# Performance work log

Hardware: AMD Instinct MI355X
Metric: run time of the kernel (lower is better)

Reference implementation:

```python
import jax, jax.numpy as jnp
import numpy as np

B, T, D = 4, 2048, 2048
P, K, ALPHA, R = 512, 16, 4, 32
E_RATIO = 0.8
EPS = 1e-6


def rmsnorm(x, g):
    return x * jax.lax.rsqrt(jnp.mean(x * x, axis=-1, keepdims=True) + EPS) * g


def dale_signs():
    # first e_ratio*P neurons excitatory (+1), rest inhibitory (-1)
    return jnp.where(jnp.arange(P) < int(E_RATIO * P), 1.0, -1.0)


def quant_dale(w, signs):
    # STE sign-quantization with per-neuron mean-abs scale + Dale's-law sign constraint
    scale = jnp.mean(jnp.abs(w), axis=-1, keepdims=True)  # [P,1]
    q = scale * signs[:, None] * jnp.ones_like(w)         # magnitude=scale, sign fixed per neuron
    return w + jax.lax.stop_gradient(q - w)


def synapse_graph(x, idx, w):
    # x: [B,T,D], idx: [P,K] int, w: [P,K] -> dendritic inputs [B,T,P,K]
    return jnp.take(x, idx, axis=-1) * w


def perceptron(x_dend, Wp, Wout, signs):
    Wq = quant_dale(Wp, signs)                              # [P,K]
    u = jnp.einsum('btpk,pk->btp', x_dend, Wq)              # [B,T,P]
    f = jax.nn.sigmoid(u)                                   # gate [B,T,P]
    f_out = quant_dale(Wout, signs)                         # [P,ALPHA]
    y = (f * u)[..., None] * f_out                          # [B,T,P,ALPHA]
    return u, f, y, f_out


def low_rank_ssm(t, f, s0, U, V, Wgate, bgate):
    # t,f: [B,T,P]; s0: [B,R]. Low-rank gated linear scan in R dims.
    z = jnp.einsum('btp,pr->btr', t, U)
    lam = jax.nn.sigmoid(jnp.einsum('btp,pr->btr', f, Wgate) + bgate)

    def step(s, inp):
        z_t, l_t = inp
        s = l_t * s + z_t
        return s, s

    sT, S = jax.lax.scan(step, s0, (jnp.moveaxis(z, 1, 0), jnp.moveaxis(lam, 1, 0)))
    tilde = jnp.einsum('btr,rp->btp', jnp.moveaxis(S, 0, 1), V)
    return tilde, sT


def flatten_ports(y):
    return y.reshape(*y.shape[:-2], P * ALPHA)


def setup_inputs() -> dict:
    key = jax.random.key(0)
    ks = jax.random.split(key, 14)
    sc = 0.1
    return {
        'x': jax.random.normal(ks[0], (B, T, D), jnp.float32),
        'state': jnp.zeros((B, R), jnp.float32),
        'g1': jnp.ones((D,), jnp.float32),
        'g2': jnp.ones((D,), jnp.float32),
        'idx_ssm': jax.random.randint(ks[1], (P, K), 0, D),
        'wg_ssm': jax.random.normal(ks[2], (P, K), jnp.float32) * sc,
        'idx_mlp': jax.random.randint(ks[3], (P, K), 0, D),
        'wg_mlp': jax.random.normal(ks[4], (P, K), jnp.float32) * sc,
        'Wp_ssm': jax.random.normal(ks[5], (P, K), jnp.float32) * sc,
        'Wout_ssm': jax.random.normal(ks[6], (P, ALPHA), jnp.float32) * sc,
        'Wp_mlp': jax.random.normal(ks[7], (P, K), jnp.float32) * sc,
        'Wout_mlp': jax.random.normal(ks[8], (P, ALPHA), jnp.float32) * sc,
        'U': jax.random.normal(ks[9], (P, R), jnp.float32) * sc,
        'V': jax.random.normal(ks[10], (R, P), jnp.float32) * sc,
        'Wgate': jax.random.normal(ks[11], (P, R), jnp.float32) * sc,
        'bgate': jnp.zeros((R,), jnp.float32),
    }


def reference(x, state, g1, g2, idx_ssm, wg_ssm, idx_mlp, wg_mlp,
              Wp_ssm, Wout_ssm, Wp_mlp, Wout_mlp, U, V, Wgate, bgate):
    signs = dale_signs()
    # --- SSM branch ---
    h1 = rmsnorm(x, g1)
    x_dend_ssm = synapse_graph(h1, idx_ssm, wg_ssm)
    u_ssm, f_ssm, _, f_out = perceptron(x_dend_ssm, Wp_ssm, Wout_ssm, signs)
    t_ssm = f_ssm * u_ssm
    tilde_t, new_state = low_rank_ssm(t_ssm, f_ssm, state, U, V, Wgate, bgate)
    y_ssm = (f_ssm * tilde_t)[..., None] * f_out            # [B,T,P,ALPHA]
    x_after = x + flatten_ports(y_ssm)
    # --- MLP branch ---
    h2 = rmsnorm(x_after, g2)
    x_dend_mlp = synapse_graph(h2, idx_mlp, wg_mlp)
    _, _, y_mlp, _ = perceptron(x_dend_mlp, Wp_mlp, Wout_mlp, signs)
    x_out = x_after + flatten_ports(y_mlp)
    return x_out, new_state
```

## Files before the change

kernel.cpp:

```cpp
#include <hip/hip_runtime.h>
#include <hip/hip_bf16.h>

#define B_ 4
#define T_ 2048
#define D_ 2048
#define P_ 512
#define K_ 16
#define ALPHA_ 4
#define R_ 32
#define NE_ 409
#define EPS_ 1e-6f
#define G_ 4

typedef unsigned short u16;
typedef unsigned int u32;
typedef _Float16 h2t __attribute__((ext_vector_type(2)));

__device__ __forceinline__ float sigmoidf_(float x) {
  return 1.0f / (1.0f + __expf(-x));
}
__device__ __forceinline__ float bfb2f(u16 u) {
  return __uint_as_float(((u32)u) << 16);
}
__device__ __forceinline__ u16 f2bfb(float f) {
  __hip_bfloat16 h = __float2bfloat16(f);
  return *reinterpret_cast<u16*>(&h);
}
__device__ __forceinline__ u32 packh(float lo, float hi) {
#if __has_builtin(__builtin_amdgcn_cvt_pkrtz)
  return __builtin_bit_cast(u32, __builtin_amdgcn_cvt_pkrtz(lo, hi));
#else
  union { _Float16 h; u16 u; } a, b;
  a.h = (_Float16)lo; b.h = (_Float16)hi;
  return ((u32)b.u << 16) | a.u;
#endif
}
__device__ __forceinline__ u32 duph(float w) {
  union { _Float16 h; u16 u; } c;
  c.h = (_Float16)w;
  return ((u32)c.u << 16) | c.u;
}
__device__ __forceinline__ h2t pkfma(u32 h, u32 w, h2t acc) {
  return __builtin_bit_cast(h2t, h) * __builtin_bit_cast(h2t, w) + acc;
}

__global__ void k_scalars(const float* __restrict__ Wp_s, const float* __restrict__ Wo_s,
                          const float* __restrict__ Wp_m, const float* __restrict__ Wo_m,
                          const float* __restrict__ U, const float* __restrict__ Wgt,
                          const float* __restrict__ wg_s, const float* __restrict__ wg_m,
                          float* __restrict__ wq_s, float* __restrict__ fo_s,
                          float* __restrict__ wq_m, float* __restrict__ fo_m,
                          u32* __restrict__ Ud, u32* __restrict__ Wd,
                          u32* __restrict__ wgd_s, u32* __restrict__ wgd_m) {
  int p = blockIdx.x * blockDim.x + threadIdx.x;
  if (p >= P_) return;
  float sgn = (p < NE_) ? 1.0f : -1.0f;
  float a = 0, b = 0, c = 0, d = 0;
#pragma unroll
  for (int k = 0; k < K_; k++) {
    a += fabsf(Wp_s[p * K_ + k]);
    c += fabsf(Wp_m[p * K_ + k]);
  }
#pragma unroll
  for (int k = 0; k < ALPHA_; k++) {
    b += fabsf(Wo_s[p * ALPHA_ + k]);
    d += fabsf(Wo_m[p * ALPHA_ + k]);
  }
  wq_s[p] = sgn * a * (1.0f / K_);
  fo_s[p] = sgn * b * (1.0f / ALPHA_);
  wq_m[p] = sgn * c * (1.0f / K_);
  fo_m[p] = sgn * d * (1.0f / ALPHA_);
#pragma unroll
  for (int r = 0; r < R_; r++) {
    Ud[p * R_ + r] = duph(U[p * R_ + r]);
    Wd[p * R_ + r] = duph(Wgt[p * R_ + r]);
  }
#pragma unroll
  for (int k = 0; k < K_; k++) {
    wgd_s[p * K_ + k] = duph(wg_s[p * K_ + k]);
    wgd_m[p * K_ + k] = duph(wg_m[p * K_ + k]);
  }
}

__global__ __launch_bounds__(512) void k_phase1(
    const float* __restrict__ x, const float* __restrict__ g1,
    const int* __restrict__ idx, const u32* __restrict__ wgd,
    const u32* __restrict__ Ud, const u32* __restrict__ Wd,
    const float* __restrict__ bg, const float* __restrict__ wq,
    u16* __restrict__ f_ssm, float* __restrict__ z, float* __restrict__ lam) {
  __shared__ union SU {
    u32 h1p[2][D_];
    struct { float zp[G_][R_][8]; float lp[G_][R_][8]; } c;
  } su;
  __shared__ u32 tp[2][P_];
  __shared__ u32 fp[2][P_];
  __shared__ float red[G_][8];

  int tid = threadIdx.x;
  int token0 = blockIdx.x * G_;
  int b = token0 >> 11;
  int t0 = token0 & (T_ - 1);

  float gv[4];
  *reinterpret_cast<float4*>(gv) = *reinterpret_cast<const float4*>(g1 + tid * 4);
#pragma unroll
  for (int pr = 0; pr < 2; pr++) {
    int ta = 2 * pr, tb = ta + 1;
    float xv0[4], xv1[4];
    *reinterpret_cast<float4*>(xv0) =
        *reinterpret_cast<const float4*>(x + (size_t)(token0 + ta) * D_ + tid * 4);
    *reinterpret_cast<float4*>(xv1) =
        *reinterpret_cast<const float4*>(x + (size_t)(token0 + tb) * D_ + tid * 4);
    float ss0 = 0, ss1 = 0;
    u32 tmp[4];
#pragma unroll
    for (int i = 0; i < 4; i++) {
      ss0 += xv0[i] * xv0[i];
      ss1 += xv1[i] * xv1[i];
      tmp[i] = packh(xv0[i] * gv[i], xv1[i] * gv[i]);
    }
    *reinterpret_cast<uint4*>(&su.h1p[pr][tid * 4]) = *reinterpret_cast<const uint4*>(tmp);
#pragma unroll
    for (int off = 32; off; off >>= 1) {
      ss0 += __shfl_down(ss0, off);
      ss1 += __shfl_down(ss1, off);
    }
    if ((tid & 63) == 0) { red[ta][tid >> 6] = ss0; red[tb][tid >> 6] = ss1; }
  }
  __syncthreads();

  float inv[G_];
#pragma unroll
  for (int tok = 0; tok < G_; tok++) {
    float s = 0;
#pragma unroll
    for (int w = 0; w < 8; w++) s += red[tok][w];
    inv[tok] = rsqrtf(s * (1.0f / D_) + EPS_);
  }

  {
    int p = tid;
    union { int4 v[4]; int s[16]; } iu;
    const int4* ip = reinterpret_cast<const int4*>(idx + p * K_);
    iu.v[0] = ip[0]; iu.v[1] = ip[1]; iu.v[2] = ip[2]; iu.v[3] = ip[3];
    union { uint4 v[4]; u32 s[16]; } wd;
    const uint4* wp = reinterpret_cast<const uint4*>(wgd + p * K_);
    wd.v[0] = wp[0]; wd.v[1] = wp[1]; wd.v[2] = wp[2]; wd.v[3] = wp[3];
    float wqp = wq[p];
#pragma unroll
    for (int pr = 0; pr < 2; pr++) {
      int ta = 2 * pr, tb = ta + 1;
      h2t acc = {(_Float16)0.0f, (_Float16)0.0f};
#pragma unroll
      for (int k = 0; k < K_; k++) acc = pkfma(su.h1p[pr][iu.s[k]], wd.s[k], acc);
      float u0 = wqp * inv[ta] * (float)acc.x, u1 = wqp * inv[tb] * (float)acc.y;
      float f0 = sigmoidf_(u0), f1 = sigmoidf_(u1);
      tp[pr][p] = packh(f0 * u0, f1 * u1);
      fp[pr][p] = packh(f0, f1);
      f_ssm[(size_t)(token0 + ta) * P_ + p] = f2bfb(f0);
      f_ssm[(size_t)(token0 + tb) * P_ + p] = f2bfb(f1);
    }
  }
  __syncthreads();

  int r = tid & 31, g = tid >> 5;
  float zs[G_] = {0, 0, 0, 0}, ls[G_] = {0, 0, 0, 0};
  int pb = g * 32;
#pragma unroll
  for (int c = 0; c < 4; c++) {
    h2t z0 = {(_Float16)0.0f, (_Float16)0.0f}, z1 = z0, l0 = z0, l1 = z0;
#pragma unroll
    for (int i = 0; i < 8; i++) {
      int p = pb + c * 8 + i;
      u32 ud = Ud[p * R_ + r];
      u32 wdd = Wd[p * R_ + r];
      z0 = pkfma(tp[0][p], ud, z0);
      z1 = pkfma(tp[1][p], ud, z1);
      l0 = pkfma(fp[0][p], wdd, l0);
      l1 = pkfma(fp[1][p], wdd, l1);
    }
    zs[0] += (float)z0.x; zs[1] += (float)z0.y; zs[2] += (float)z1.x; zs[3] += (float)z1.y;
    ls[0] += (float)l0.x; ls[1] += (float)l0.y; ls[2] += (float)l1.x; ls[3] += (float)l1.y;
  }
#pragma unroll
  for (int tok = 0; tok < G_; tok++) {
    zs[tok] += __shfl_down(zs[tok], 32);
    ls[tok] += __shfl_down(ls[tok], 32);
  }
  int wid = tid >> 6;
  if ((tid & 63) < 32) {
#pragma unroll
    for (int tok = 0; tok < G_; tok++) { su.c.zp[tok][r][wid] = zs[tok]; su.c.lp[tok][r][wid] = ls[tok]; }
  }
  __syncthreads();
  if (tid < R_) {
    float bgr = bg[tid];
    float z4[G_], l4[G_];
#pragma unroll
    for (int tok = 0; tok < G_; tok++) {
      float zz = 0, ll = 0;
#pragma unroll
      for (int w = 0; w < 8; w++) { zz += su.c.zp[tok][tid][w]; ll += su.c.lp[tok][tid][w]; }
      z4[tok] = zz;
      l4[tok] = sigmoidf_(ll + bgr);
    }
    size_t o = ((size_t)(b * R_ + tid)) * T_ + t0;
    *reinterpret_cast<float4*>(&z[o]) = *reinterpret_cast<const float4*>(z4);
    *reinterpret_cast<float4*>(&lam[o]) = *reinterpret_cast<const float4*>(l4);
  }
}

__global__ __launch_bounds__(64) void k_scan(
    const float* __restrict__ z, const float* __restrict__ lam,
    const float* __restrict__ state, float* __restrict__ S,
    float* __restrict__ out_state) {
  int br = blockIdx.x;
  int lane = threadIdx.x;
  const float* zr = z + (size_t)br * T_ + lane * 32;
  const float* lr = lam + (size_t)br * T_ + lane * 32;
  float zb[32], lb[32];
#pragma unroll
  for (int i = 0; i < 32; i += 4) {
    *reinterpret_cast<float4*>(&zb[i]) = *reinterpret_cast<const float4*>(&zr[i]);
    *reinterpret_cast<float4*>(&lb[i]) = *reinterpret_cast<const float4*>(&lr[i]);
  }
  float A = 1.0f, Z = 0.0f;
#pragma unroll
  for (int i = 0; i < 32; i++) { Z = lb[i] * Z + zb[i]; A *= lb[i]; }
  for (int off = 1; off < 64; off <<= 1) {
    float Ap = __shfl_up(A, off);
    float Zp = __shfl_up(Z, off);
    if (lane >= off) { Z = A * Zp + Z; A = A * Ap; }
  }
  float s0 = state[br];
  float Ae = __shfl_up(A, 1);
  float Ze = __shfl_up(Z, 1);
  float s = (lane == 0) ? s0 : (Ae * s0 + Ze);
  float sb[32];
#pragma unroll
  for (int i = 0; i < 32; i++) { s = lb[i] * s + zb[i]; sb[i] = s; }
  float* Sr = S + (size_t)br * T_ + lane * 32;
#pragma unroll
  for (int i = 0; i < 32; i += 4)
    *reinterpret_cast<float4*>(&Sr[i]) = *reinterpret_cast<const float4*>(&sb[i]);
  if (lane == 63) out_state[br] = s;
}

__global__ __launch_bounds__(512) void k_phase3(
    const float* __restrict__ x, const float* __restrict__ g2,
    const int* __restrict__ idx, const u32* __restrict__ wgd,
    const float* __restrict__ V, const float* __restrict__ S,
    const u16* __restrict__ f_ssm, const float* __restrict__ fo_s,
    const float* __restrict__ wq_m, const float* __restrict__ fo_m,
    float* __restrict__ out) {
  __shared__ float Sl[G_][R_];
  __shared__ u32 h2p[2][D_];
  __shared__ float red[G_][8];

  int tid = threadIdx.x;
  int token0 = blockIdx.x * G_;
  int b = token0 >> 11;
  int t0 = token0 & (T_ - 1);
  int p = tid;

  if (tid < G_ * R_) {
    int tok = tid >> 5, r = tid & 31;
    Sl[tok][r] = S[((size_t)(b * R_ + r)) * T_ + t0 + tok];
  }
  __syncthreads();

  float til[G_] = {0, 0, 0, 0};
#pragma unroll 4
  for (int r = 0; r < R_; r++) {
    float v = V[r * P_ + p];
#pragma unroll
    for (int tok = 0; tok < G_; tok++) til[tok] += Sl[tok][r] * v;
  }

  float fo = fo_s[p];
  float gv[4];
  *reinterpret_cast<float4*>(gv) = *reinterpret_cast<const float4*>(g2 + tid * 4);

  float xa[G_][4];
#pragma unroll
  for (int pr = 0; pr < 2; pr++) {
    int ta = 2 * pr, tb = ta + 1;
#pragma unroll
    for (int h = 0; h < 2; h++) {
      int tok = ta + h;
      float fv = bfb2f(f_ssm[(size_t)(token0 + tok) * P_ + p]);
      float val = fv * til[tok] * fo;
      float xv[4];
      *reinterpret_cast<float4*>(xv) =
          *reinterpret_cast<const float4*>(x + (size_t)(token0 + tok) * D_ + tid * 4);
      float ss = 0;
#pragma unroll
      for (int a = 0; a < 4; a++) {
        float v = xv[a] + val;
        xa[tok][a] = v;
        ss += v * v;
      }
#pragma unroll
      for (int off = 32; off; off >>= 1) ss += __shfl_down(ss, off);
      if ((tid & 63) == 0) red[tok][tid >> 6] = ss;
    }
    u32 tmp[4];
#pragma unroll
    for (int i = 0; i < 4; i++)
      tmp[i] = packh(xa[ta][i] * gv[i], xa[tb][i] * gv[i]);
    *reinterpret_cast<uint4*>(&h2p[pr][tid * 4]) = *reinterpret_cast<const uint4*>(tmp);
  }
  __syncthreads();

  float invt[G_];
#pragma unroll
  for (int tok = 0; tok < G_; tok++) {
    float s = 0;
#pragma unroll
    for (int w = 0; w < 8; w++) s += red[tok][w];
    invt[tok] = rsqrtf(s * (1.0f / D_) + EPS_);
  }

  union { int4 v[4]; int s[16]; } iu;
  union { uint4 v[4]; u32 s[16]; } wd;
  {
    const int4* ip = reinterpret_cast<const int4*>(idx + p * K_);
    const uint4* wp = reinterpret_cast<const uint4*>(wgd + p * K_);
#pragma unroll
    for (int q = 0; q < 4; q++) { iu.v[q] = ip[q]; wd.v[q] = wp[q]; }
  }
  float wqm = wq_m[p];
  float fom = fo_m[p];

#pragma unroll
  for (int pr = 0; pr < 2; pr++) {
    h2t acc = {(_Float16)0.0f, (_Float16)0.0f};
#pragma unroll
    for (int k = 0; k < K_; k++) acc = pkfma(h2p[pr][iu.s[k]], wd.s[k], acc);
#pragma unroll
    for (int h = 0; h < 2; h++) {
      int tok = 2 * pr + h;
      float a = h ? (float)acc.y : (float)acc.x;
      float u = wqm * invt[tok] * a;
      float f = sigmoidf_(u);
      float val = f * u * fom;
      float ov[4];
#pragma unroll
      for (int a2 = 0; a2 < 4; a2++) ov[a2] = xa[tok][a2] + val;
      *reinterpret_cast<float4*>(out + (size_t)(token0 + tok) * D_ + tid * 4) =
          *reinterpret_cast<const float4*>(ov);
    }
  }
}

extern "C" void kernel_launch(void* const* d_in, const int* in_sizes, int n_in,
                              void* d_out, int out_size, void* d_ws, size_t ws_size,
                              hipStream_t stream) {
  const float* x     = (const float*)d_in[0];
  const float* state = (const float*)d_in[1];
  const float* g1    = (const float*)d_in[2];
  const float* g2    = (const float*)d_in[3];
  const int*   idx_s = (const int*)d_in[4];
  const float* wg_s  = (const float*)d_in[5];
  const int*   idx_m = (const int*)d_in[6];
  const float* wg_m  = (const float*)d_in[7];
  const float* Wp_s  = (const float*)d_in[8];
  const float* Wo_s  = (const float*)d_in[9];
  const float* Wp_m  = (const float*)d_in[10];
  const float* Wo_m  = (const float*)d_in[11];
  const float* U     = (const float*)d_in[12];
  const float* V     = (const float*)d_in[13];
  const float* Wgt   = (const float*)d_in[14];
  const float* bg    = (const float*)d_in[15];
  float* out = (float*)d_out;

  char* ws = (char*)d_ws;
  float* wq_s = (float*)(ws + 0);
  float* fo_s = (float*)(ws + 2048);
  float* wq_m = (float*)(ws + 4096);
  float* fo_m = (float*)(ws + 6144);
  u32* Ud     = (u32*)(ws + 8192);
  u32* Wd     = (u32*)(ws + 8192 + 65536);
  u32* wgd_s  = (u32*)(ws + 8192 + 131072);
  u32* wgd_m  = (u32*)(ws + 8192 + 163840);
  size_t off = 8192 + 196608;
  u16* f_ssm = (u16*)(ws + off); off += (size_t)B_ * T_ * P_ * 2;
  float* z   = (float*)(ws + off); off += (size_t)B_ * R_ * T_ * 4;
  float* lam = (float*)(ws + off); off += (size_t)B_ * R_ * T_ * 4;
  float* S   = (float*)(ws + off);

  hipLaunchKernelGGL(k_scalars, dim3(2), dim3(256), 0, stream,
                     Wp_s, Wo_s, Wp_m, Wo_m, U, Wgt, wg_s, wg_m,
                     wq_s, fo_s, wq_m, fo_m, Ud, Wd, wgd_s, wgd_m);
  hipLaunchKernelGGL(k_phase1, dim3(B_ * T_ / G_), dim3(512), 0, stream,
                     x, g1, idx_s, wgd_s, Ud, Wd, bg, wq_s, f_ssm, z, lam);
  hipLaunchKernelGGL(k_scan, dim3(B_ * R_), dim3(64), 0, stream,
                     z, lam, state, S, out + (size_t)B_ * T_ * D_);
  hipLaunchKernelGGL(k_phase3, dim3(B_ * T_ / G_), dim3(512), 0, stream,
                     x, g2, idx_m, wgd_m, V, S, f_ssm, fo_s, wq_m, fo_m, out);
}
```

Baseline: 207.6 us.

## Store f_ssm as packed fp16 pairs, hoist index loads, vectorize LDS reads

The SSM gate f is now stored as one packed fp16 pair per token pair (one 32-bit store) instead of two scattered bf16 stores, and phase3 reads it back as a single word. Index and scale loads are hoisted to kernel start in both phases so their latency overlaps the RMSnorm reductions. The low-rank projection reads tp/fp from LDS with 128-bit loads, and both kernels get a min-blocks launch bound. The aim is fewer global transactions and better latency hiding. The costs are fp16 rounding of f instead of bf16 and added register pressure from the bound.

After: 223.3 us. +7.6%, slower.

```diff
diff --git a/kernel.cpp b/kernel.cpp
--- a/kernel.cpp
+++ b/kernel.cpp
@@ -19,13 +19,6 @@
 __device__ __forceinline__ float sigmoidf_(float x) {
   return 1.0f / (1.0f + __expf(-x));
 }
-__device__ __forceinline__ float bfb2f(u16 u) {
-  return __uint_as_float(((u32)u) << 16);
-}
-__device__ __forceinline__ u16 f2bfb(float f) {
-  __hip_bfloat16 h = __float2bfloat16(f);
-  return *reinterpret_cast<u16*>(&h);
-}
 __device__ __forceinline__ u32 packh(float lo, float hi) {
 #if __has_builtin(__builtin_amdgcn_cvt_pkrtz)
   return __builtin_bit_cast(u32, __builtin_amdgcn_cvt_pkrtz(lo, hi));
@@ -35,6 +28,8 @@
   return ((u32)b.u << 16) | a.u;
 #endif
 }
+__device__ __forceinline__ float hlo(u32 u) { return (float)__builtin_bit_cast(h2t, u).x; }
+__device__ __forceinline__ float hhi(u32 u) { return (float)__builtin_bit_cast(h2t, u).y; }
 __device__ __forceinline__ u32 duph(float w) {
   union { _Float16 h; u16 u; } c;
   c.h = (_Float16)w;
@@ -82,12 +77,12 @@
   }
 }
 
-__global__ __launch_bounds__(512) void k_phase1(
+__global__ __launch_bounds__(512, 8) void k_phase1(
     const float* __restrict__ x, const float* __restrict__ g1,
     const int* __restrict__ idx, const u32* __restrict__ wgd,
     const u32* __restrict__ Ud, const u32* __restrict__ Wd,
     const float* __restrict__ bg, const float* __restrict__ wq,
-    u16* __restrict__ f_ssm, float* __restrict__ z, float* __restrict__ lam) {
+    u32* __restrict__ f_ssm, float* __restrict__ z, float* __restrict__ lam) {
   __shared__ union SU {
     u32 h1p[2][D_];
     struct { float zp[G_][R_][8]; float lp[G_][R_][8]; } c;
@@ -100,6 +95,13 @@
   int token0 = blockIdx.x * G_;
   int b = token0 >> 11;
   int t0 = token0 & (T_ - 1);
+
+  union { int4 v[4]; int s[16]; } iu;
+  {
+    const int4* ip = reinterpret_cast<const int4*>(idx + tid * K_);
+    iu.v[0] = ip[0]; iu.v[1] = ip[1]; iu.v[2] = ip[2]; iu.v[3] = ip[3];
+  }
+  float wqp = wq[tid];
 
   float gv[4];
   *reinterpret_cast<float4*>(gv) = *reinterpret_cast<const float4*>(g1 + tid * 4);
@@ -140,13 +142,9 @@
 
   {
     int p = tid;
-    union { int4 v[4]; int s[16]; } iu;
-    const int4* ip = reinterpret_cast<const int4*>(idx + p * K_);
-    iu.v[0] = ip[0]; iu.v[1] = ip[1]; iu.v[2] = ip[2]; iu.v[3] = ip[3];
     union { uint4 v[4]; u32 s[16]; } wd;
     const uint4* wp = reinterpret_cast<const uint4*>(wgd + p * K_);
     wd.v[0] = wp[0]; wd.v[1] = wp[1]; wd.v[2] = wp[2]; wd.v[3] = wp[3];
-    float wqp = wq[p];
 #pragma unroll
     for (int pr = 0; pr < 2; pr++) {
       int ta = 2 * pr, tb = ta + 1;
@@ -156,9 +154,9 @@
       float u0 = wqp * inv[ta] * (float)acc.x, u1 = wqp * inv[tb] * (float)acc.y;
       float f0 = sigmoidf_(u0), f1 = sigmoidf_(u1);
       tp[pr][p] = packh(f0 * u0, f1 * u1);
-      fp[pr][p] = packh(f0, f1);
-      f_ssm[(size_t)(token0 + ta) * P_ + p] = f2bfb(f0);
-      f_ssm[(size_t)(token0 + tb) * P_ + p] = f2bfb(f1);
+      u32 fpk = packh(f0, f1);
+      fp[pr][p] = fpk;
+      f_ssm[(size_t)(2 * blockIdx.x + pr) * P_ + p] = fpk;
     }
   }
   __syncthreads();
@@ -170,14 +168,20 @@
   for (int c = 0; c < 4; c++) {
     h2t z0 = {(_Float16)0.0f, (_Float16)0.0f}, z1 = z0, l0 = z0, l1 = z0;
 #pragma unroll
-    for (int i = 0; i < 8; i++) {
-      int p = pb + c * 8 + i;
-      u32 ud = Ud[p * R_ + r];
-      u32 wdd = Wd[p * R_ + r];
-      z0 = pkfma(tp[0][p], ud, z0);
-      z1 = pkfma(tp[1][p], ud, z1);
-      l0 = pkfma(fp[0][p], wdd, l0);
-      l1 = pkfma(fp[1][p], wdd, l1);
+    for (int q = 0; q < 2; q++) {
+      int p = pb + c * 8 + q * 4;
+      uint4 t0 = *reinterpret_cast<const uint4*>(&tp[0][p]);
+      uint4 t1 = *reinterpret_cast<const uint4*>(&tp[1][p]);
+      uint4 f0 = *reinterpret_cast<const uint4*>(&fp[0][p]);
+      uint4 f1 = *reinterpret_cast<const uint4*>(&fp[1][p]);
+      u32 u0 = Ud[(p + 0) * R_ + r], u1 = Ud[(p + 1) * R_ + r];
+      u32 u2 = Ud[(p + 2) * R_ + r], u3 = Ud[(p + 3) * R_ + r];
+      u32 w0 = Wd[(p + 0) * R_ + r], w1 = Wd[(p + 1) * R_ + r];
+      u32 w2 = Wd[(p + 2) * R_ + r], w3 = Wd[(p + 3) * R_ + r];
+      z0 = pkfma(t0.w, u3, pkfma(t0.z, u2, pkfma(t0.y, u1, pkfma(t0.x, u0, z0))));
+      z1 = pkfma(t1.w, u3, pkfma(t1.z, u2, pkfma(t1.y, u1, pkfma(t1.x, u0, z1))));
+      l0 = pkfma(f0.w, w3, pkfma(f0.z, w2, pkfma(f0.y, w1, pkfma(f0.x, w0, l0))));
+      l1 = pkfma(f1.w, w3, pkfma(f1.z, w2, pkfma(f1.y, w1, pkfma(f1.x, w0, l1))));
     }
     zs[0] += (float)z0.x; zs[1] += (float)z0.y; zs[2] += (float)z1.x; zs[3] += (float)z1.y;
     ls[0] += (float)l0.x; ls[1] += (float)l0.y; ls[2] += (float)l1.x; ls[3] += (float)l1.y;
@@ -246,11 +250,11 @@
   if (lane == 63) out_state[br] = s;
 }
 
-__global__ __launch_bounds__(512) void k_phase3(
+__global__ __launch_bounds__(512, 8) void k_phase3(
     const float* __restrict__ x, const float* __restrict__ g2,
     const int* __restrict__ idx, const u32* __restrict__ wgd,
     const float* __restrict__ V, const float* __restrict__ S,
-    const u16* __restrict__ f_ssm, const float* __restrict__ fo_s,
+    const u32* __restrict__ f_ssm, const float* __restrict__ fo_s,
     const float* __restrict__ wq_m, const float* __restrict__ fo_m,
     float* __restrict__ out) {
   __shared__ float Sl[G_][R_];
@@ -263,6 +267,16 @@
   int t0 = token0 & (T_ - 1);
   int p = tid;
 
+  union { int4 v[4]; int s[16]; } iu;
+  {
+    const int4* ip = reinterpret_cast<const int4*>(idx + p * K_);
+    iu.v[0] = ip[0]; iu.v[1] = ip[1]; iu.v[2] = ip[2]; iu.v[3] = ip[3];
+  }
+  u32 fw[2];
+#pragma unroll
+  for (int pr = 0; pr < 2; pr++)
+    fw[pr] = f_ssm[(size_t)(2 * blockIdx.x + pr) * P_ + p];
+
   if (tid < G_ * R_) {
     int tok = tid >> 5, r = tid & 31;
     Sl[tok][r] = S[((size_t)(b * R_ + r)) * T_ + t0 + tok];
@@ -288,7 +302,7 @@
 #pragma unroll
     for (int h = 0; h < 2; h++) {
       int tok = ta + h;
-      float fv = bfb2f(f_ssm[(size_t)(token0 + tok) * P_ + p]);
+      float fv = h ? hhi(fw[pr]) : hlo(fw[pr]);
       float val = fv * til[tok] * fo;
       float xv[4];
       *reinterpret_cast<float4*>(xv) =
@@ -321,13 +335,11 @@
     invt[tok] = rsqrtf(s * (1.0f / D_) + EPS_);
   }
 
-  union { int4 v[4]; int s[16]; } iu;
   union { uint4 v[4]; u32 s[16]; } wd;
   {
-    const int4* ip = reinterpret_cast<const int4*>(idx + p * K_);
     const uint4* wp = reinterpret_cast<const uint4*>(wgd + p * K_);
 #pragma unroll
-    for (int q = 0; q < 4; q++) { iu.v[q] = ip[q]; wd.v[q] = wp[q]; }
+    for (int q = 0; q < 4; q++) wd.v[q] = wp[q];
   }
   float wqm = wq_m[p];
   float fom = fo_m[p];
@@ -384,7 +396,7 @@
   u32* wgd_s  = (u32*)(ws + 8192 + 131072);
   u32* wgd_m  = (u32*)(ws + 8192 + 163840);
   size_t off = 8192 + 196608;
-  u16* f_ssm = (u16*)(ws + off); off += (size_t)B_ * T_ * P_ * 2;
+  u32* f_ssm = (u32*)(ws + off); off += (size_t)(B_ * T_ / 2) * P_ * 4;
   float* z   = (float*)(ws + off); off += (size_t)B_ * R_ * T_ * 4;
   float* lam = (float*)(ws + off); off += (size_t)B_ * R_ * T_ * 4;
   float* S   = (float*)(ws + off);
```
